# Kernel optimization log

Measured on AMD Instinct MI355X. Metric: run time of the kernel, lower is better.

The kernel has to match this reference:

```python
import jax, jax.numpy as jnp
import numpy as np

N_QUBITS = 4
NOISE_RATE = 0.01  # depolarizing channel scales Pauli-Z expectation by (1 - p)


def _rx_mat(theta):
    # RX(theta) = [[cos(t/2), -i sin(t/2)], [-i sin(t/2), cos(t/2)]]; theta scalar or (b,)
    c = jnp.cos(theta / 2).astype(jnp.complex64)
    s = (-1j * jnp.sin(theta / 2)).astype(jnp.complex64)
    return jnp.stack([jnp.stack([c, s], -1), jnp.stack([s, c], -1)], -2)


def _apply_1q(state, mat, wire):
    # state: (b, 2,2,2,2); mat: (2,2) shared or (b,2,2) per-sample
    st = jnp.moveaxis(state, wire + 1, -1)
    if mat.ndim == 2:
        st = st @ mat.T
    else:
        st = jnp.einsum('b...j,bij->b...i', st, mat)
    return jnp.moveaxis(st, -1, wire + 1)


def _cnot(state, src, tgt):
    st = jnp.moveaxis(state, (src + 1, tgt + 1), (-2, -1))
    st = jnp.concatenate([st[..., 0:1, :], st[..., 1:2, ::-1]], axis=-2)
    return jnp.moveaxis(st, (-2, -1), (src + 1, tgt + 1))


def _qlayer(x, theta):
    # x: (b, n_qubits) encoding angles; theta: (n_params,) trainable RX angles
    b = x.shape[0]
    state = jnp.zeros((b,) + (2,) * N_QUBITS, jnp.complex64)
    state = state.at[(slice(None),) + (0,) * N_QUBITS].set(1.0)
    for w in range(N_QUBITS):                      # GeneralEncoder: RX(x_w) on wire w
        state = _apply_1q(state, _rx_mat(x[:, w]), w)
    for k in range(theta.shape[0]):                # trainable RX_k on wire k
        state = _apply_1q(state, _rx_mat(theta[k]), k)
    for i in range(N_QUBITS):                      # CNOT ring (i, (i+1)%n)
        state = _cnot(state, i, (i + 1) % N_QUBITS)
    p = jnp.abs(state) ** 2                        # (b, 2,2,2,2)
    ez = []
    for w in range(N_QUBITS):                      # <Z_w> = P(0) - P(1)
        axes = tuple(a for a in range(1, N_QUBITS + 1) if a != w + 1)
        m = p.sum(axes)
        ez.append(m[:, 0] - m[:, 1])
    return (1.0 - NOISE_RATE) * jnp.stack(ez, -1)  # depolarizing noise on expectations


def reference(inputs, w_lin, b_lin, w_map, b_map, theta):
    # inputs: (S, B, D); gate order: forget, input, update, output
    S, B, D = inputs.shape
    H = w_map.shape[1]
    hx0 = jnp.zeros((B, H), inputs.dtype)
    cx0 = jnp.zeros((B, H), inputs.dtype)
    qbatch = jax.vmap(_qlayer)  # over the 4 gates

    def step(carry, x):
        hx, cx = carry
        comb = jnp.concatenate([x, hx], axis=1)                      # (B, D+H)
        pre = jnp.einsum('gqd,bd->gbq', w_lin, comb) + b_lin[:, None, :]
        q = qbatch(pre, theta)                                       # (4, B, n_qubits)
        acts = jnp.stack([jax.nn.sigmoid(q[0]), jax.nn.sigmoid(q[1]),
                          jnp.tanh(q[2]), jax.nn.sigmoid(q[3])])
        gates = jnp.einsum('ghq,gbq->gbh', w_map, acts) + b_map[:, None, :]
        f, i_, g, o = gates
        cx2 = f * cx + i_ * g
        hx2 = o * jnp.tanh(cx2)
        return (hx2, cx2), hx2

    (hx, cx), outputs = jax.lax.scan(step, (hx0, cx0), inputs)
    return outputs, hx, cx


def setup_inputs() -> dict:
    key = jax.random.key(0)
    ks = jax.random.split(key, 6)
    S, B, D, H, NQ, NG = 512, 256, 128, 256, 4, 4
    return {
        'inputs': jax.random.normal(ks[0], (S, B, D), jnp.float32),
        'w_lin': jax.random.normal(ks[1], (NG, NQ, D + H), jnp.float32) * 0.05,
        'b_lin': jax.random.normal(ks[2], (NG, NQ), jnp.float32) * 0.05,
        'w_map': jax.random.normal(ks[3], (NG, H, NQ), jnp.float32) * 0.3,
        'b_map': jax.random.normal(ks[4], (NG, H), jnp.float32) * 0.05,
        'theta': jax.random.uniform(ks[5], (NG, 4), jnp.float32, 0.0, 2.0 * np.pi),
    }
```

## Files before the change

kernel.cpp:

```cpp
#include <hip/hip_runtime.h>

#define SEQ   512
#define BATCH 256
#define DIN   128
#define HID   256
#define NOISE 0.99f

__device__ __forceinline__ float dot4(float4 a, float4 b) {
    return fmaf(a.x, b.x, fmaf(a.y, b.y, fmaf(a.z, b.z, a.w * b.w)));
}
__device__ __forceinline__ float sigmoid_(float x) {
    return 1.0f / (1.0f + __expf(-x));
}
__device__ __forceinline__ float tanh_(float x) {
    float ax = fabsf(x);
    float e  = __expf(2.0f * ax);
    float r  = 1.0f - 2.0f / (e + 1.0f);
    return copysignf(r, x);
}

template <int CTRL>
__device__ __forceinline__ float dppmov(float v) {
    return __int_as_float(__builtin_amdgcn_mov_dpp(__float_as_int(v), CTRL, 0xF, 0xF, false));
}
__device__ __forceinline__ float swap16_sum(float v) {
    float a = v, b;
    asm("v_mov_b32 %1, %0\n\tv_permlane16_swap_b32 %0, %1" : "+v"(a), "=&v"(b));
    return a + b;
}
__device__ __forceinline__ float swap32_sum(float v) {
    float a = v, b;
    asm("v_mov_b32 %1, %0\n\tv_permlane32_swap_b32 %0, %1" : "+v"(a), "=&v"(b));
    return a + b;
}

__global__ __launch_bounds__(256, 2) void pre_gemm(
    const float* __restrict__ x,
    const float* __restrict__ w_lin,
    const float* __restrict__ b_lin,
    const float* __restrict__ theta,
    float* pre, int pstride)
{
    __shared__ float wlds[16 * 132];
    const int t = threadIdx.x;
    for (int i = t; i < 16 * 128; i += 256) {
        int pp = i >> 7, dd = i & 127;
        wlds[pp * 132 + dd] = w_lin[pp * 384 + dd];
    }
    __syncthreads();
    const int s = blockIdx.x >> 4;
    const int b = ((blockIdx.x & 15) << 4) + (t >> 4);
    const int p = t & 15;
    const float* xr = x + ((size_t)s * BATCH + b) * DIN;
    const float* wr = &wlds[p * 132];
    float acc = b_lin[p] + theta[p];
    #pragma unroll 8
    for (int d = 0; d < 32; ++d)
        acc += dot4(*(const float4*)(xr + d * 4), *(const float4*)(wr + d * 4));
    pre[((size_t)s * BATCH + b) * pstride + p] = acc;
}

__global__ __launch_bounds__(256, 1) void qlstm_rec(
    const float* __restrict__ w_lin,
    const float* __restrict__ w_map,
    const float* __restrict__ b_map,
    const float* pre, int pstride,
    float* out)
{
    const int b = blockIdx.x;
    const int t = threadIdx.x;
    const int l = t & 63;
    const int g = t >> 6;
    const int q = l & 3;
    const int j = l >> 2;
    const int p = (g << 2) | q;

    __shared__ __align__(16) float hx_lds[HID];
    __shared__ __align__(16) float acts_lds[16];

    const int sig = (j >> 1) & 3;
    const float* wp = w_lin + p * 384 + 128 + j * 16;
    const float4 wh0 = *(const float4*)(wp + ((0 ^ sig) << 2));
    const float4 wh1 = *(const float4*)(wp + ((1 ^ sig) << 2));
    const float4 wh2 = *(const float4*)(wp + ((2 ^ sig) << 2));
    const float4 wh3 = *(const float4*)(wp + ((3 ^ sig) << 2));

    const float4 wm0 = ((const float4*)w_map)[0 * 256 + t];
    const float4 wm1 = ((const float4*)w_map)[1 * 256 + t];
    const float4 wm2 = ((const float4*)w_map)[2 * 256 + t];
    const float4 wm3 = ((const float4*)w_map)[3 * 256 + t];
    const float bm0 = b_map[t];
    const float bm1 = b_map[256 + t];
    const float bm2 = b_map[512 + t];
    const float bm3 = b_map[768 + t];

    const float* hr = &hx_lds[j * 16];
    const float* hr0 = hr + ((0 ^ sig) << 2);
    const float* hr1 = hr + ((1 ^ sig) << 2);
    const float* hr2 = hr + ((2 ^ sig) << 2);
    const float* hr3 = hr + ((3 ^ sig) << 2);

    const float*  pb      = pre + (size_t)b * pstride + p;
    const size_t  sstride = (size_t)BATCH * pstride;
    float px0 = pb[0];
    float px1 = pb[sstride];

    hx_lds[t] = 0.0f;
    float hx = 0.0f, cx = 0.0f;
    float* out_seq = out;
    float* out_hx  = out + (size_t)SEQ * BATCH * HID;
    float* out_cx  = out_hx + BATCH * HID;
    __syncthreads();

    for (int s = 0; s < SEQ; ++s) {
        const float pxu = px0;
        px0 = px1;
        const int s2 = (s + 2 < SEQ) ? s + 2 : SEQ - 1;
        px1 = pb[(size_t)s2 * sstride];

        const float4 ha0 = *(const float4*)hr0;
        const float4 ha1 = *(const float4*)hr1;
        const float4 ha2 = *(const float4*)hr2;
        const float4 ha3 = *(const float4*)hr3;
        float acc = dot4(wh0, ha0) + dot4(wh1, ha1)
                  + dot4(wh2, ha2) + dot4(wh3, ha3);
        acc += dppmov<0x124>(acc);
        acc += dppmov<0x128>(acc);
        acc  = swap16_sum(acc);
        acc  = swap32_sum(acc);

        const float A  = __cosf(acc + pxu);
        const float Bv = dppmov<0xB1>(A);
        const float Cv = dppmov<0x4E>(A);
        const float Dv = dppmov<0x4E>(Bv);

        const float t1 = Cv * Dv;
        const float u  = (q & 1) ? (A * Bv) : ((q == 2) ? A : Bv);
        const float v  = (q == 1) ? 1.0f : t1;
        const float ez = NOISE * u * v;
        const float act = (g == 2) ? tanh_(ez) : sigmoid_(ez);
        if (l < 4) acts_lds[(g << 2) | l] = act;
        __syncthreads();

        const float4 a0 = *(const float4*)&acts_lds[0];
        const float4 a1 = *(const float4*)&acts_lds[4];
        const float4 a2 = *(const float4*)&acts_lds[8];
        const float4 a3 = *(const float4*)&acts_lds[12];

        const float fv = bm0 + dot4(wm0, a0);
        const float iv = bm1 + dot4(wm1, a1);
        const float gv = bm2 + dot4(wm2, a2);
        const float ov = bm3 + dot4(wm3, a3);

        cx = fmaf(fv, cx, iv * gv);
        hx = ov * tanh_(cx);

        hx_lds[t] = hx;
        out_seq[((size_t)s * BATCH + b) * HID + t] = hx;
        __syncthreads();
    }

    out_hx[(size_t)b * HID + t] = hx;
    out_cx[(size_t)b * HID + t] = cx;
}

extern "C" void kernel_launch(void* const* d_in, const int* in_sizes, int n_in,
                              void* d_out, int out_size, void* d_ws, size_t ws_size,
                              hipStream_t stream) {
    const float* x     = (const float*)d_in[0];
    const float* w_lin = (const float*)d_in[1];
    const float* b_lin = (const float*)d_in[2];
    const float* w_map = (const float*)d_in[3];
    const float* b_map = (const float*)d_in[4];
    const float* theta = (const float*)d_in[5];
    float* out = (float*)d_out;

    const size_t pre_bytes = (size_t)SEQ * BATCH * 16 * sizeof(float);
    float* pre;
    int pstride;
    if (ws_size >= pre_bytes) {
        pre = (float*)d_ws;
        pstride = 16;
    } else {
        pre = out;
        pstride = HID;
    }

    pre_gemm<<<dim3(SEQ * 16), dim3(256), 0, stream>>>(x, w_lin, b_lin, theta, pre, pstride);
    qlstm_rec<<<dim3(BATCH), dim3(256), 0, stream>>>(w_lin, w_map, b_map, pre, pstride, out);
}
```

Measured before the change: 297.3 us.

## Run recurrent QLSTM step in a single wavefront with DPP/readlane exchange

Measured after the change: 444.5 us. +49.5%, slower.

```diff
diff --git a/kernel.cpp b/kernel.cpp
--- a/kernel.cpp
+++ b/kernel.cpp
@@ -4,13 +4,9 @@
 #define BATCH 256
 #define DIN   128
 #define HID   256
-#define NOISE 0.99f
 
 __device__ __forceinline__ float dot4(float4 a, float4 b) {
     return fmaf(a.x, b.x, fmaf(a.y, b.y, fmaf(a.z, b.z, a.w * b.w)));
-}
-__device__ __forceinline__ float sigmoid_(float x) {
-    return 1.0f / (1.0f + __expf(-x));
 }
 __device__ __forceinline__ float tanh_(float x) {
     float ax = fabsf(x);
@@ -18,10 +14,13 @@
     float r  = 1.0f - 2.0f / (e + 1.0f);
     return copysignf(r, x);
 }
-
 template <int CTRL>
-__device__ __forceinline__ float dppmov(float v) {
+__device__ __forceinline__ float dppf(float v) {
     return __int_as_float(__builtin_amdgcn_mov_dpp(__float_as_int(v), CTRL, 0xF, 0xF, false));
+}
+template <int CTRL>
+__device__ __forceinline__ float4 dpp4(float4 v) {
+    return make_float4(dppf<CTRL>(v.x), dppf<CTRL>(v.y), dppf<CTRL>(v.z), dppf<CTRL>(v.w));
 }
 __device__ __forceinline__ float swap16_sum(float v) {
     float a = v, b;
@@ -33,8 +32,11 @@
     asm("v_mov_b32 %1, %0\n\tv_permlane32_swap_b32 %0, %1" : "+v"(a), "=&v"(b));
     return a + b;
 }
-
-__global__ __launch_bounds__(256, 2) void pre_gemm(
+__device__ __forceinline__ float rdlanef(float v, int lane) {
+    return __int_as_float(__builtin_amdgcn_readlane(__float_as_int(v), lane));
+}
+
+__global__ __launch_bounds__(256, 4) void pre_gemm(
     const float* __restrict__ x,
     const float* __restrict__ w_lin,
     const float* __restrict__ b_lin,
@@ -60,7 +62,7 @@
     pre[((size_t)s * BATCH + b) * pstride + p] = acc;
 }
 
-__global__ __launch_bounds__(256, 1) void qlstm_rec(
+__global__ __launch_bounds__(64, 1) void qlstm_rec(
     const float* __restrict__ w_lin,
     const float* __restrict__ w_map,
     const float* __restrict__ b_map,
@@ -68,100 +70,123 @@
     float* out)
 {
     const int b = blockIdx.x;
-    const int t = threadIdx.x;
-    const int l = t & 63;
-    const int g = t >> 6;
-    const int q = l & 3;
-    const int j = l >> 2;
-    const int p = (g << 2) | q;
-
-    __shared__ __align__(16) float hx_lds[HID];
-    __shared__ __align__(16) float acts_lds[16];
-
-    const int sig = (j >> 1) & 3;
-    const float* wp = w_lin + p * 384 + 128 + j * 16;
-    const float4 wh0 = *(const float4*)(wp + ((0 ^ sig) << 2));
-    const float4 wh1 = *(const float4*)(wp + ((1 ^ sig) << 2));
-    const float4 wh2 = *(const float4*)(wp + ((2 ^ sig) << 2));
-    const float4 wh3 = *(const float4*)(wp + ((3 ^ sig) << 2));
-
-    const float4 wm0 = ((const float4*)w_map)[0 * 256 + t];
-    const float4 wm1 = ((const float4*)w_map)[1 * 256 + t];
-    const float4 wm2 = ((const float4*)w_map)[2 * 256 + t];
-    const float4 wm3 = ((const float4*)w_map)[3 * 256 + t];
-    const float bm0 = b_map[t];
-    const float bm1 = b_map[256 + t];
-    const float bm2 = b_map[512 + t];
-    const float bm3 = b_map[768 + t];
-
-    const float* hr = &hx_lds[j * 16];
-    const float* hr0 = hr + ((0 ^ sig) << 2);
-    const float* hr1 = hr + ((1 ^ sig) << 2);
-    const float* hr2 = hr + ((2 ^ sig) << 2);
-    const float* hr3 = hr + ((3 ^ sig) << 2);
-
-    const float*  pb      = pre + (size_t)b * pstride + p;
-    const size_t  sstride = (size_t)BATCH * pstride;
-    float px0 = pb[0];
-    float px1 = pb[sstride];
-
-    hx_lds[t] = 0.0f;
-    float hx = 0.0f, cx = 0.0f;
-    float* out_seq = out;
-    float* out_hx  = out + (size_t)SEQ * BATCH * HID;
-    float* out_cx  = out_hx + BATCH * HID;
-    __syncthreads();
+    const int l = threadIdx.x;
+    const int a = l & 3;
+    const int Q = l >> 2;
+    const bool sg1 = (Q >> 1) & 1;
+    const bool sg2 = (Q >> 2) & 1;
+    const bool isT = (a == 2);
+
+    float4 wh4[4][4];
+    #pragma unroll
+    for (int q = 0; q < 4; ++q)
+        #pragma unroll
+        for (int c = 0; c < 4; ++c)
+            wh4[q][c] = *(const float4*)(w_lin + (4*a + q) * 384 + 128 + 16*Q + 4*c);
+
+    float4 wm[4][4];
+    float  bmv[4][4];
+    #pragma unroll
+    for (int g2 = 0; g2 < 4; ++g2) {
+        #pragma unroll
+        for (int m = 0; m < 4; ++m)
+            wm[g2][m] = *(const float4*)(w_map + ((size_t)(g2 * 256 + 4*l + m)) * 4);
+        float4 bq = *(const float4*)(b_map + g2 * 256 + 4*l);
+        bmv[g2][0] = bq.x; bmv[g2][1] = bq.y; bmv[g2][2] = bq.z; bmv[g2][3] = bq.w;
+    }
+
+    const float nm = isT ? 2.0f : 1.0f;
+
+    const float* pb = pre + (size_t)b * pstride + 4*a;
+    const size_t sstride = (size_t)BATCH * pstride;
+    float4 px0 = *(const float4*)(pb);
+    float4 px1 = *(const float4*)(pb + sstride);
+
+    float4 hxv = make_float4(0.f, 0.f, 0.f, 0.f);
+    float  cxa[4] = {0.f, 0.f, 0.f, 0.f};
+
+    float* outp   = out + (size_t)b * HID + 4*l;
+    float* out_hx = out + (size_t)SEQ * BATCH * HID;
+    float* out_cx = out_hx + BATCH * HID;
 
     for (int s = 0; s < SEQ; ++s) {
-        const float pxu = px0;
+        const float4 pcur = px0;
         px0 = px1;
-        const int s2 = (s + 2 < SEQ) ? s + 2 : SEQ - 1;
-        px1 = pb[(size_t)s2 * sstride];
-
-        const float4 ha0 = *(const float4*)hr0;
-        const float4 ha1 = *(const float4*)hr1;
-        const float4 ha2 = *(const float4*)hr2;
-        const float4 ha3 = *(const float4*)hr3;
-        float acc = dot4(wh0, ha0) + dot4(wh1, ha1)
-                  + dot4(wh2, ha2) + dot4(wh3, ha3);
-        acc += dppmov<0x124>(acc);
-        acc += dppmov<0x128>(acc);
-        acc  = swap16_sum(acc);
-        acc  = swap32_sum(acc);
-
-        const float A  = __cosf(acc + pxu);
-        const float Bv = dppmov<0xB1>(A);
-        const float Cv = dppmov<0x4E>(A);
-        const float Dv = dppmov<0x4E>(Bv);
-
-        const float t1 = Cv * Dv;
-        const float u  = (q & 1) ? (A * Bv) : ((q == 2) ? A : Bv);
-        const float v  = (q == 1) ? 1.0f : t1;
-        const float ez = NOISE * u * v;
-        const float act = (g == 2) ? tanh_(ez) : sigmoid_(ez);
-        if (l < 4) acts_lds[(g << 2) | l] = act;
-        __syncthreads();
-
-        const float4 a0 = *(const float4*)&acts_lds[0];
-        const float4 a1 = *(const float4*)&acts_lds[4];
-        const float4 a2 = *(const float4*)&acts_lds[8];
-        const float4 a3 = *(const float4*)&acts_lds[12];
-
-        const float fv = bm0 + dot4(wm0, a0);
-        const float iv = bm1 + dot4(wm1, a1);
-        const float gv = bm2 + dot4(wm2, a2);
-        const float ov = bm3 + dot4(wm3, a3);
-
-        cx = fmaf(fv, cx, iv * gv);
-        hx = ov * tanh_(cx);
-
-        hx_lds[t] = hx;
-        out_seq[((size_t)s * BATCH + b) * HID + t] = hx;
-        __syncthreads();
-    }
-
-    out_hx[(size_t)b * HID + t] = hx;
-    out_cx[(size_t)b * HID + t] = cx;
+        const int s2 = (s + 2 < SEQ) ? (s + 2) : (SEQ - 1);
+        px1 = *(const float4*)(pb + (size_t)s2 * sstride);
+
+        const float4 h0 = dpp4<0x00>(hxv);
+        const float4 h1 = dpp4<0x55>(hxv);
+        const float4 h2 = dpp4<0xAA>(hxv);
+        const float4 h3 = dpp4<0xFF>(hxv);
+
+        float pq[4];
+        #pragma unroll
+        for (int q = 0; q < 4; ++q) {
+            const float d0 = dot4(wh4[q][0], h0);
+            const float d1 = dot4(wh4[q][1], h1);
+            const float d2 = dot4(wh4[q][2], h2);
+            const float d3 = dot4(wh4[q][3], h3);
+            const float A01 = d0 + d1;
+            const float A23 = d2 + d3;
+            const float t1 = sg2 ? A23 : A01;
+            const float u  = sg2 ? (sg1 ? d1 : d0) : (sg1 ? d3 : d2);
+            const float w  = sg2 ? (sg1 ? d0 : d1) : (sg1 ? d2 : d3);
+            float v = (t1 + u) + w;
+            v += dppf<0x124>(v);
+            v += dppf<0x128>(v);
+            v  = swap16_sum(v);
+            v  = swap32_sum(v);
+            pq[q] = v;
+        }
+
+        const float A0 = __cosf(pq[0] + pcur.x);
+        const float A1 = __cosf(pq[1] + pcur.y);
+        const float A2 = __cosf(pq[2] + pcur.z);
+        const float A3 = __cosf(pq[3] + pcur.w);
+
+        const float s01 = A0 * A1;
+        const float s23 = A2 * A3;
+        const float ezv[4] = {
+            (0.99f * A1)  * s23,
+            (0.99f * s01) * 1.0f,
+            (0.99f * A2)  * s01,
+            (0.99f * s23) * s01
+        };
+
+        float act[4];
+        #pragma unroll
+        for (int q = 0; q < 4; ++q) {
+            const float z   = ezv[q];
+            const float arg = isT ? 2.0f * fabsf(z) : -z;
+            const float E   = __expf(arg);
+            const float dd  = nm / (E + 1.0f);
+            act[q] = isT ? copysignf(1.0f - dd, z) : dd;
+        }
+
+        const float4 AR0 = make_float4(rdlanef(act[0],0), rdlanef(act[1],0), rdlanef(act[2],0), rdlanef(act[3],0));
+        const float4 AR1 = make_float4(rdlanef(act[0],1), rdlanef(act[1],1), rdlanef(act[2],1), rdlanef(act[3],1));
+        const float4 AR2 = make_float4(rdlanef(act[0],2), rdlanef(act[1],2), rdlanef(act[2],2), rdlanef(act[3],2));
+        const float4 AR3 = make_float4(rdlanef(act[0],3), rdlanef(act[1],3), rdlanef(act[2],3), rdlanef(act[3],3));
+
+        float hxa[4];
+        #pragma unroll
+        for (int m = 0; m < 4; ++m) {
+            const float fv = bmv[0][m] + dot4(wm[0][m], AR0);
+            const float iv = bmv[1][m] + dot4(wm[1][m], AR1);
+            const float gv = bmv[2][m] + dot4(wm[2][m], AR2);
+            const float ov = bmv[3][m] + dot4(wm[3][m], AR3);
+            cxa[m] = fmaf(fv, cxa[m], iv * gv);
+            hxa[m] = ov * tanh_(cxa[m]);
+        }
+        hxv = make_float4(hxa[0], hxa[1], hxa[2], hxa[3]);
+
+        *(float4*)outp = hxv;
+        outp += (size_t)BATCH * HID;
+    }
+
+    *(float4*)(out_hx + (size_t)b * HID + 4*l) = hxv;
+    *(float4*)(out_cx + (size_t)b * HID + 4*l) = make_float4(cxa[0], cxa[1], cxa[2], cxa[3]);
 }
 
 extern "C" void kernel_launch(void* const* d_in, const int* in_sizes, int n_in,
@@ -187,5 +212,5 @@
     }
 
     pre_gemm<<<dim3(SEQ * 16), dim3(256), 0, stream>>>(x, w_lin, b_lin, theta, pre, pstride);
-    qlstm_rec<<<dim3(BATCH), dim3(256), 0, stream>>>(w_lin, w_map, b_map, pre, pstride, out);
-}
+    qlstm_rec<<<dim3(BATCH), dim3(64), 0, stream>>>(w_lin, w_map, b_map, pre, pstride, out);
+}
```

## Compute all gate activations redundantly per wave to drop mid-step barrier

Applied to the files above, without the earlier changes.

Measured after the change: 425.3 us. 43.1% more time.

```diff
diff --git a/kernel.cpp b/kernel.cpp
--- a/kernel.cpp
+++ b/kernel.cpp
@@ -18,9 +18,8 @@
     float r  = 1.0f - 2.0f / (e + 1.0f);
     return copysignf(r, x);
 }
-
 template <int CTRL>
-__device__ __forceinline__ float dppmov(float v) {
+__device__ __forceinline__ float dppf(float v) {
     return __int_as_float(__builtin_amdgcn_mov_dpp(__float_as_int(v), CTRL, 0xF, 0xF, false));
 }
 __device__ __forceinline__ float swap16_sum(float v) {
@@ -33,8 +32,11 @@
     asm("v_mov_b32 %1, %0\n\tv_permlane32_swap_b32 %0, %1" : "+v"(a), "=&v"(b));
     return a + b;
 }
-
-__global__ __launch_bounds__(256, 2) void pre_gemm(
+__device__ __forceinline__ float rdlanef(float v, int lane) {
+    return __int_as_float(__builtin_amdgcn_readlane(__float_as_int(v), lane));
+}
+
+__global__ __launch_bounds__(256, 4) void pre_gemm(
     const float* __restrict__ x,
     const float* __restrict__ w_lin,
     const float* __restrict__ b_lin,
@@ -70,20 +72,18 @@
     const int b = blockIdx.x;
     const int t = threadIdx.x;
     const int l = t & 63;
-    const int g = t >> 6;
     const int q = l & 3;
     const int j = l >> 2;
-    const int p = (g << 2) | q;
-
-    __shared__ __align__(16) float hx_lds[HID];
-    __shared__ __align__(16) float acts_lds[16];
-
     const int sig = (j >> 1) & 3;
-    const float* wp = w_lin + p * 384 + 128 + j * 16;
-    const float4 wh0 = *(const float4*)(wp + ((0 ^ sig) << 2));
-    const float4 wh1 = *(const float4*)(wp + ((1 ^ sig) << 2));
-    const float4 wh2 = *(const float4*)(wp + ((2 ^ sig) << 2));
-    const float4 wh3 = *(const float4*)(wp + ((3 ^ sig) << 2));
+
+    __shared__ __align__(16) float hx_lds[2][HID];
+
+    float4 wh[4][4];
+    #pragma unroll
+    for (int gg = 0; gg < 4; ++gg)
+        #pragma unroll
+        for (int k = 0; k < 4; ++k)
+            wh[gg][k] = *(const float4*)(w_lin + ((gg << 2) | q) * 384 + 128 + j * 16 + ((k ^ sig) << 2));
 
     const float4 wm0 = ((const float4*)w_map)[0 * 256 + t];
     const float4 wm1 = ((const float4*)w_map)[1 * 256 + t];
@@ -94,18 +94,22 @@
     const float bm2 = b_map[512 + t];
     const float bm3 = b_map[768 + t];
 
-    const float* hr = &hx_lds[j * 16];
-    const float* hr0 = hr + ((0 ^ sig) << 2);
-    const float* hr1 = hr + ((1 ^ sig) << 2);
-    const float* hr2 = hr + ((2 ^ sig) << 2);
-    const float* hr3 = hr + ((3 ^ sig) << 2);
-
-    const float*  pb      = pre + (size_t)b * pstride + p;
-    const size_t  sstride = (size_t)BATCH * pstride;
-    float px0 = pb[0];
-    float px1 = pb[sstride];
-
-    hx_lds[t] = 0.0f;
+    const int o0 = j * 16 + ((0 ^ sig) << 2);
+    const int o1 = j * 16 + ((1 ^ sig) << 2);
+    const int o2 = j * 16 + ((2 ^ sig) << 2);
+    const int o3 = j * 16 + ((3 ^ sig) << 2);
+
+    const size_t sstride = (size_t)BATCH * pstride;
+    const float* pb[4];
+    float px0[4], px1[4];
+    #pragma unroll
+    for (int gg = 0; gg < 4; ++gg) {
+        pb[gg]  = pre + (size_t)b * pstride + ((gg << 2) | q);
+        px0[gg] = pb[gg][0];
+        px1[gg] = pb[gg][sstride];
+    }
+
+    hx_lds[0][t] = 0.0f;
     float hx = 0.0f, cx = 0.0f;
     float* out_seq = out;
     float* out_hx  = out + (size_t)SEQ * BATCH * HID;
@@ -113,49 +117,56 @@
     __syncthreads();
 
     for (int s = 0; s < SEQ; ++s) {
-        const float pxu = px0;
-        px0 = px1;
         const int s2 = (s + 2 < SEQ) ? s + 2 : SEQ - 1;
-        px1 = pb[(size_t)s2 * sstride];
-
-        const float4 ha0 = *(const float4*)hr0;
-        const float4 ha1 = *(const float4*)hr1;
-        const float4 ha2 = *(const float4*)hr2;
-        const float4 ha3 = *(const float4*)hr3;
-        float acc = dot4(wh0, ha0) + dot4(wh1, ha1)
-                  + dot4(wh2, ha2) + dot4(wh3, ha3);
-        acc += dppmov<0x124>(acc);
-        acc += dppmov<0x128>(acc);
-        acc  = swap16_sum(acc);
-        acc  = swap32_sum(acc);
-
-        const float A  = __cosf(acc + pxu);
-        const float Bv = dppmov<0xB1>(A);
-        const float Cv = dppmov<0x4E>(A);
-        const float Dv = dppmov<0x4E>(Bv);
-
-        const float t1 = Cv * Dv;
-        const float u  = (q & 1) ? (A * Bv) : ((q == 2) ? A : Bv);
-        const float v  = (q == 1) ? 1.0f : t1;
-        const float ez = NOISE * u * v;
-        const float act = (g == 2) ? tanh_(ez) : sigmoid_(ez);
-        if (l < 4) acts_lds[(g << 2) | l] = act;
-        __syncthreads();
-
-        const float4 a0 = *(const float4*)&acts_lds[0];
-        const float4 a1 = *(const float4*)&acts_lds[4];
-        const float4 a2 = *(const float4*)&acts_lds[8];
-        const float4 a3 = *(const float4*)&acts_lds[12];
-
-        const float fv = bm0 + dot4(wm0, a0);
-        const float iv = bm1 + dot4(wm1, a1);
-        const float gv = bm2 + dot4(wm2, a2);
-        const float ov = bm3 + dot4(wm3, a3);
+
+        const float* hb = hx_lds[s & 1];
+        const float4 ha0 = *(const float4*)(hb + o0);
+        const float4 ha1 = *(const float4*)(hb + o1);
+        const float4 ha2 = *(const float4*)(hb + o2);
+        const float4 ha3 = *(const float4*)(hb + o3);
+
+        float actg[4];
+        #pragma unroll
+        for (int gg = 0; gg < 4; ++gg) {
+            float acc = dot4(wh[gg][0], ha0) + dot4(wh[gg][1], ha1)
+                      + dot4(wh[gg][2], ha2) + dot4(wh[gg][3], ha3);
+            acc += dppf<0x124>(acc);
+            acc += dppf<0x128>(acc);
+            acc  = swap16_sum(acc);
+            acc  = swap32_sum(acc);
+
+            const float pxu = px0[gg];
+            px0[gg] = px1[gg];
+            px1[gg] = pb[gg][(size_t)s2 * sstride];
+
+            const float A  = __cosf(acc + pxu);
+            const float Bv = dppf<0xB1>(A);
+            const float Cv = dppf<0x4E>(A);
+            const float Dv = dppf<0x4E>(Bv);
+
+            const float t1 = Cv * Dv;
+            const float u  = (q & 1) ? (A * Bv) : ((q == 2) ? A : Bv);
+            const float v  = (q == 1) ? 1.0f : t1;
+            const float ez = NOISE * u * v;
+            actg[gg] = (gg == 2) ? tanh_(ez) : sigmoid_(ez);
+        }
+
+        float ar[4][4];
+        #pragma unroll
+        for (int gg = 0; gg < 4; ++gg)
+            #pragma unroll
+            for (int qq = 0; qq < 4; ++qq)
+                ar[gg][qq] = rdlanef(actg[gg], qq);
+
+        const float fv = bm0 + fmaf(wm0.x, ar[0][0], fmaf(wm0.y, ar[0][1], fmaf(wm0.z, ar[0][2], wm0.w * ar[0][3])));
+        const float iv = bm1 + fmaf(wm1.x, ar[1][0], fmaf(wm1.y, ar[1][1], fmaf(wm1.z, ar[1][2], wm1.w * ar[1][3])));
+        const float gv = bm2 + fmaf(wm2.x, ar[2][0], fmaf(wm2.y, ar[2][1], fmaf(wm2.z, ar[2][2], wm2.w * ar[2][3])));
+        const float ov = bm3 + fmaf(wm3.x, ar[3][0], fmaf(wm3.y, ar[3][1], fmaf(wm3.z, ar[3][2], wm3.w * ar[3][3])));
 
         cx = fmaf(fv, cx, iv * gv);
         hx = ov * tanh_(cx);
 
-        hx_lds[t] = hx;
+        hx_lds[(s + 1) & 1][t] = hx;
         out_seq[((size_t)s * BATCH + b) * HID + t] = hx;
         __syncthreads();
     }
```
